# Optimization experiments

Hardware: AMD Instinct MI355X
Metric: run time of the kernel (lower is better)

Reference implementation:

```python
import jax, jax.numpy as jnp
from jax import lax
import numpy as np

NUM_TOKENS = 2048
HIDDEN = 768
MAX_SPAN_WIDTH = 20
NUM_CAND = NUM_TOKENS * MAX_SPAN_WIDTH  # 40960
FEAT = 20
UNARY = 1024
SPAN_DIM = 3 * HIDDEN + FEAT  # 2324
MAX_NUM_SPANS = 512
TOP_SPAN_RATIO = 0.4


def setup_inputs() -> dict:
    key = jax.random.key(0)
    ks = jax.random.split(key, 16)
    starts = jax.random.randint(ks[0], (NUM_CAND,), 0, NUM_TOKENS, dtype=jnp.int32)
    widths = jax.random.randint(ks[1], (NUM_CAND,), 0, MAX_SPAN_WIDTH, dtype=jnp.int32)
    ends = jnp.minimum(starts + widths, NUM_TOKENS - 1)
    p = lambda k, shp: (0.02 * jax.random.normal(k, shp, dtype=jnp.float32))
    return {
        "hidden_states": jax.random.normal(ks[2], (NUM_TOKENS, HIDDEN), dtype=jnp.float32),
        "candidate_starts": starts,
        "candidate_ends": ends,
        "speaker_ids": jax.random.randint(ks[3], (NUM_TOKENS,), 0, 2, dtype=jnp.int32),
        "w_attn": p(ks[4], (HIDDEN,)),
        "b_attn": p(ks[5], ()),
        "W1": p(ks[6], (SPAN_DIM, UNARY)),
        "b1": p(ks[7], (UNARY,)),
        "W2": p(ks[8], (UNARY,)),
        "b2": p(ks[9], ()),
        "emb_width": p(ks[10], (MAX_SPAN_WIDTH, FEAT)),
        "emb_width_prior": p(ks[11], (MAX_SPAN_WIDTH, FEAT)),
        "Wp1": p(ks[12], (FEAT, UNARY)),
        "bp1": p(ks[13], (UNARY,)),
        "Wp2": p(ks[14], (UNARY,)),
        "bp2": p(ks[15], ()),
    }


def extract_spans(starts, ends, scores, num_top, num_words):
    """Greedy NMS-style span pruning: take spans by descending score, rejecting
    spans that partially overlap (cross) an already-accepted span; return
    num_top accepted candidate indices sorted by (start, end)."""
    order = jnp.argsort(-scores)  # descending score
    s_sorted = starts[order]
    e_sorted = ends[order]
    tok = jnp.arange(num_words, dtype=jnp.int32)

    def step(carry, se):
        latest_end, earliest_start, count = carry
        s, e = se
        in_range = (tok >= s) & (tok <= e)
        cross = jnp.any(in_range & (tok > s) & (latest_end > e)) | \
                jnp.any(in_range & (tok < e) & (earliest_start < s))
        accept = jnp.logical_and(~cross, count < num_top)
        latest_end = jnp.where(accept, latest_end.at[s].max(e), latest_end)
        earliest_start = jnp.where(accept, earliest_start.at[e].min(s), earliest_start)
        count = count + accept.astype(jnp.int32)
        return (latest_end, earliest_start, count), accept

    init = (jnp.full((num_words,), -1, jnp.int32),
            jnp.full((num_words,), num_words, jnp.int32),
            jnp.int32(0))
    (_, _, count), accepted = lax.scan(step, init, (s_sorted, e_sorted))
    # sort accepted spans by (start, end); push rejected to the back
    BIG = jnp.int32(np.iinfo(np.int32).max)
    sort_key = jnp.where(accepted, s_sorted * (num_words + 1) + e_sorted, BIG)
    by_pos = jnp.argsort(sort_key)
    picked = order[by_pos[:num_top]]
    # pad (if fewer than num_top accepted) with the first accepted span
    valid = jnp.arange(num_top) < count
    return jnp.where(valid, picked, picked[0])


def reference(hidden_states, candidate_starts, candidate_ends, speaker_ids,
              w_attn, b_attn, W1, b1, W2, b2,
              emb_width, emb_width_prior, Wp1, bp1, Wp2, bp2):
    num_words = hidden_states.shape[0]
    num_top_spans = int(min(MAX_NUM_SPANS, num_words * TOP_SPAN_RATIO))

    # masked softmax attention pooling over each span's tokens
    tok_att = hidden_states @ w_attn + b_attn            # [T]
    doc = jnp.arange(num_words, dtype=jnp.int32)
    token_mask = (doc[None, :] >= candidate_starts[:, None]) & \
                 (doc[None, :] <= candidate_ends[:, None])  # [C, T]
    logits = jnp.where(token_mask, tok_att[None, :], -jnp.inf)
    token_attn = jax.nn.softmax(logits, axis=1)          # [C, T]
    attended = token_attn @ hidden_states                # [C, H]

    width_idx = candidate_ends - candidate_starts        # in [0, MAX_SPAN_WIDTH)
    span_emb = jnp.concatenate([
        hidden_states[candidate_starts],
        hidden_states[candidate_ends],
        emb_width[width_idx],
        attended,
    ], axis=1)                                           # [C, 3H+F]

    h = jax.nn.relu(span_emb @ W1 + b1)
    span_scores = h @ W2 + b2                            # [C]
    hp = jax.nn.relu(emb_width_prior[width_idx] @ Wp1 + bp1)
    span_scores = span_scores + (hp @ Wp2 + bp2)

    pruned_idx = extract_spans(candidate_starts, candidate_ends,
                               lax.stop_gradient(span_scores),
                               num_top_spans, num_words)
    pruned_starts = candidate_starts[pruned_idx]
    pruned_ends = candidate_ends[pruned_idx]
    pruned_emb = span_emb[pruned_idx]
    pruned_scores = span_scores[pruned_idx]
    pruned_speaker_ids = speaker_ids[pruned_starts]
    return (span_emb, pruned_idx, pruned_starts, pruned_ends,
            pruned_emb, pruned_scores, pruned_speaker_ids)
```

## Files before the change

kernel.cpp:

```cpp
#include <hip/hip_runtime.h>
#include <math.h>

#define NT 2048
#define HID 768
#define NC 40960
#define NFEAT 20
#define UN 1024
#define SDIM 2324
#define NTOP 512
#define WMAX 20

#define OFF_IDX   95191040
#define OFF_S     95191552
#define OFF_E     95192064
#define OFF_PEMB  95192576
#define OFF_SC    96382464
#define OFF_SP    96382976

__global__ void k_zero(int* __restrict__ p, int n) {
  int i = blockIdx.x * 256 + threadIdx.x;
  if (i < n) p[i] = 0;
}

__global__ void k_hist(const int* __restrict__ starts, int* __restrict__ hist) {
  int i = blockIdx.x * 256 + threadIdx.x;
  atomicAdd(&hist[starts[i]], 1);
}

__global__ __launch_bounds__(256) void k_prefix(const int* __restrict__ hist,
                                                int* __restrict__ cursor) {
  __shared__ int tsum[256];
  int tid = threadIdx.x;
  int v[8], pre[8];
  int s = 0;
  #pragma unroll
  for (int j = 0; j < 8; ++j) { v[j] = hist[tid * 8 + j]; pre[j] = s; s += v[j]; }
  tsum[tid] = s;
  __syncthreads();
  for (int off = 1; off < 256; off <<= 1) {
    int t = (tid >= off) ? tsum[tid - off] : 0;
    __syncthreads();
    tsum[tid] += t;
    __syncthreads();
  }
  int base = (tid > 0) ? tsum[tid - 1] : 0;
  #pragma unroll
  for (int j = 0; j < 8; ++j) cursor[tid * 8 + j] = base + pre[j];
}

__global__ void k_place(const int* __restrict__ starts, int* __restrict__ cursor,
                        int* __restrict__ ord) {
  int i = blockIdx.x * 256 + threadIdx.x;
  int pos = atomicAdd(&cursor[starts[i]], 1);
  ord[pos] = i;
}

__global__ __launch_bounds__(256) void k_tok_att(const float* __restrict__ hidden,
                                                 const float* __restrict__ w_attn,
                                                 const float* __restrict__ b_attn,
                                                 float* __restrict__ tok_att) {
  int wave = (blockIdx.x * blockDim.x + threadIdx.x) >> 6;
  int lane = threadIdx.x & 63;
  if (wave >= NT) return;
  const float* row = hidden + (size_t)wave * HID;
  float s = 0.f;
  for (int c = lane; c < HID; c += 64) s += row[c] * w_attn[c];
  #pragma unroll
  for (int off = 32; off; off >>= 1) s += __shfl_down(s, off);
  if (lane == 0) tok_att[wave] = s + b_attn[0];
}

__global__ __launch_bounds__(256) void k_pc(const float* __restrict__ emb_width,
                                            const float* __restrict__ W1,
                                            float* __restrict__ Pc) {
  int idx = blockIdx.x * 256 + threadIdx.x;
  int w = idx >> 10, j = idx & 1023;
  float s = 0.f;
  #pragma unroll
  for (int k = 0; k < NFEAT; ++k) s += emb_width[w * NFEAT + k] * W1[(size_t)(2 * HID + k) * UN + j];
  Pc[idx] = s;
}

__global__ __launch_bounds__(256) void k_prior(const float* __restrict__ ewp,
                                               const float* __restrict__ Wp1,
                                               const float* __restrict__ bp1,
                                               const float* __restrict__ Wp2,
                                               const float* __restrict__ bp2,
                                               float* __restrict__ prior) {
  int w = blockIdx.x;
  int tid = threadIdx.x;
  __shared__ float red[256];
  float local = 0.f;
  for (int j = tid; j < UN; j += 256) {
    float hp = bp1[j];
    #pragma unroll
    for (int k = 0; k < NFEAT; ++k) hp += ewp[w * NFEAT + k] * Wp1[k * UN + j];
    local += fmaxf(hp, 0.f) * Wp2[j];
  }
  red[tid] = local;
  __syncthreads();
  for (int st = 128; st > 0; st >>= 1) { if (tid < st) red[tid] += red[tid + st]; __syncthreads(); }
  if (tid == 0) prior[w] = red[0] + bp2[0];
}

__global__ __launch_bounds__(256) void k_matmul_P(const float* __restrict__ hidden,
                                                  const float* __restrict__ W1,
                                                  float* __restrict__ P) {
  __shared__ float As[16][132];
  __shared__ float Bs[16][128];
  int bn = blockIdx.x, bm = blockIdx.y;
  int n0 = bn * 128;
  int seg = n0 >> 10;
  int rowbase = (seg == 0) ? 0 : (seg == 1 ? HID : (2 * HID + NFEAT));
  int j0 = n0 & 1023;
  int tid = threadIdx.x;
  int tx = tid & 15, ty = tid >> 4;
  float acc[8][8] = {};
  for (int k0 = 0; k0 < HID; k0 += 16) {
    #pragma unroll
    for (int q = 0; q < 2; ++q) {
      int idx = q * 256 + tid;
      int m = idx >> 2, kg = idx & 3;
      float4 a = *(const float4*)&hidden[(size_t)(bm * 128 + m) * HID + k0 + kg * 4];
      As[kg * 4 + 0][m] = a.x; As[kg * 4 + 1][m] = a.y;
      As[kg * 4 + 2][m] = a.z; As[kg * 4 + 3][m] = a.w;
      int k = idx >> 5, ng = idx & 31;
      float4 b = *(const float4*)&W1[(size_t)(rowbase + k0 + k) * UN + j0 + ng * 4];
      *(float4*)&Bs[k][ng * 4] = b;
    }
    __syncthreads();
    #pragma unroll
    for (int k = 0; k < 16; ++k) {
      float4 a0 = *(const float4*)&As[k][ty * 8];
      float4 a1 = *(const float4*)&As[k][ty * 8 + 4];
      float4 b0 = *(const float4*)&Bs[k][tx * 8];
      float4 b1 = *(const float4*)&Bs[k][tx * 8 + 4];
      float av[8] = {a0.x, a0.y, a0.z, a0.w, a1.x, a1.y, a1.z, a1.w};
      float bv[8] = {b0.x, b0.y, b0.z, b0.w, b1.x, b1.y, b1.z, b1.w};
      #pragma unroll
      for (int i = 0; i < 8; ++i)
        #pragma unroll
        for (int jj = 0; jj < 8; ++jj) acc[i][jj] += av[i] * bv[jj];
    }
    __syncthreads();
  }
  #pragma unroll
  for (int i = 0; i < 8; ++i) {
    float* prow = &P[(size_t)(bm * 128 + ty * 8 + i) * 3072 + n0 + tx * 8];
    *(float4*)prow = make_float4(acc[i][0], acc[i][1], acc[i][2], acc[i][3]);
    *(float4*)(prow + 4) = make_float4(acc[i][4], acc[i][5], acc[i][6], acc[i][7]);
  }
}

__global__ __launch_bounds__(256) void k_span(
    const int* __restrict__ ord,
    const float* __restrict__ hidden, const int* __restrict__ starts, const int* __restrict__ ends,
    const float* __restrict__ tok_att, const float* __restrict__ emb_width,
    const float* __restrict__ P, const float* __restrict__ Pc,
    const float* __restrict__ b1, const float* __restrict__ W2,
    const float* __restrict__ b2ptr, const float* __restrict__ prior,
    float* __restrict__ out, float* __restrict__ scores, unsigned long long* __restrict__ keys) {
  int i = ord[blockIdx.x];
  int s = starts[i], e = ends[i];
  int w = e - s;
  int L = w + 1;
  int tid = threadIdx.x;
  __shared__ float alpha[WMAX];
  __shared__ float red[256];
  if (tid < 64) {
    float v = (tid < L) ? tok_att[s + tid] : -3.0e38f;
    float m = v;
    #pragma unroll
    for (int off = 32; off; off >>= 1) m = fmaxf(m, __shfl_xor(m, off));
    float ex = (tid < L) ? expf(v - m) : 0.0f;
    float sum = ex;
    #pragma unroll
    for (int off = 32; off; off >>= 1) sum += __shfl_xor(sum, off);
    if (tid < L) alpha[tid] = ex / sum;
  }
  __syncthreads();
  const float* hs = hidden + (size_t)s * HID;
  const float* he = hidden + (size_t)e * HID;
  float* orow = out + (size_t)i * SDIM;
  for (int q = tid; q < SDIM / 4; q += 256) {
    int c = q * 4;
    float4 v;
    if (c < HID) v = *(const float4*)(hs + c);
    else if (c < 2 * HID) v = *(const float4*)(he + (c - HID));
    else if (c < 2 * HID + NFEAT) v = *(const float4*)(emb_width + w * NFEAT + (c - 2 * HID));
    else {
      int cc = c - (2 * HID + NFEAT);
      float ax = 0, ay = 0, az = 0, aw = 0;
      for (int t = 0; t < L; ++t) {
        float a = alpha[t];
        float4 hv = *(const float4*)(hidden + (size_t)(s + t) * HID + cc);
        ax += a * hv.x; ay += a * hv.y; az += a * hv.z; aw += a * hv.w;
      }
      v = make_float4(ax, ay, az, aw);
    }
    *(float4*)(orow + c) = v;
  }
  int j = tid * 4;
  float4 pre = *(const float4*)(b1 + j);
  float4 pa = *(const float4*)(P + (size_t)s * 3072 + j);
  float4 pb = *(const float4*)(P + (size_t)e * 3072 + 1024 + j);
  float4 pc = *(const float4*)(Pc + w * UN + j);
  pre.x += pa.x + pb.x + pc.x;
  pre.y += pa.y + pb.y + pc.y;
  pre.z += pa.z + pb.z + pc.z;
  pre.w += pa.w + pb.w + pc.w;
  for (int t = 0; t < L; ++t) {
    float a = alpha[t];
    float4 pd = *(const float4*)(P + (size_t)(s + t) * 3072 + 2048 + j);
    pre.x += a * pd.x; pre.y += a * pd.y; pre.z += a * pd.z; pre.w += a * pd.w;
  }
  float4 w2 = *(const float4*)(W2 + j);
  float local = fmaxf(pre.x, 0.f) * w2.x + fmaxf(pre.y, 0.f) * w2.y +
                fmaxf(pre.z, 0.f) * w2.z + fmaxf(pre.w, 0.f) * w2.w;
  red[tid] = local;
  __syncthreads();
  for (int st = 128; st > 0; st >>= 1) { if (tid < st) red[tid] += red[tid + st]; __syncthreads(); }
  if (tid == 0) {
    float sc = red[0] + b2ptr[0] + prior[w];
    scores[i] = sc;
    unsigned u = __float_as_uint(sc);
    u = (u >> 31) ? ~u : (u | 0x80000000u);
    unsigned inv = ~u;
    keys[i] = (((unsigned long long)inv) << 32) | (unsigned)i;
  }
}

__global__ __launch_bounds__(256) void k_rank(const unsigned long long* __restrict__ keys,
                                              int* __restrict__ rank) {
  int ic = blockIdx.x >> 5;
  int jc = blockIdx.x & 31;
  int tid = threadIdx.x;
  int ibase = ic * 2048 + tid;
  unsigned long long mk[8];
  int cnt[8];
  #pragma unroll
  for (int k = 0; k < 8; ++k) { mk[k] = keys[ibase + k * 256]; cnt[k] = 0; }
  int j0 = jc * 1280;
  #pragma unroll 4
  for (int j = j0; j < j0 + 1280; ++j) {
    unsigned long long kj = keys[j];
    #pragma unroll
    for (int k = 0; k < 8; ++k) cnt[k] += (kj < mk[k]) ? 1 : 0;
  }
  #pragma unroll
  for (int k = 0; k < 8; ++k) if (cnt[k]) atomicAdd(&rank[ibase + k * 256], cnt[k]);
}

__global__ void k_scatter(const int* __restrict__ rank, int* __restrict__ order) {
  int i = blockIdx.x * 256 + threadIdx.x;
  order[rank[i]] = i;
}

__global__ void k_scan(const int* __restrict__ order,
                       const int* __restrict__ starts,
                       const int* __restrict__ ends,
                       int* __restrict__ acc_idx, int* __restrict__ acc_s,
                       int* __restrict__ acc_e, int* __restrict__ acc_count) {
  __shared__ int LE[NT];
  __shared__ int ES[NT];
  int lane = threadIdx.x;
  for (int t = lane; t < NT; t += 64) { LE[t] = -1; ES[t] = NT; }
  __syncthreads();
  int count = 0;
  for (int base = 0; base < NC && count < NTOP; base += 64) {
    int ci = order[base + lane];
    int sv = starts[ci];
    int ev = ends[ci];
    bool pc = false;
    for (int t = sv; t <= ev; ++t) {
      int l = LE[t], es2 = ES[t];
      pc = pc || ((t > sv) && (l > ev)) || ((t < ev) && (es2 < sv));
    }
    unsigned long long pm = __ballot(pc);
    int localCount = 0;
    int ls = 0, le = -1, li = 0;
    for (int t = 0; t < 64; ++t) {
      int s = __shfl(sv, t);
      int e = __shfl(ev, t);
      int cidx = __shfl(ci, t);
      bool ov = (lane < localCount) &&
                (((s < ls) && (ls <= e) && (e < le)) ||
                 ((ls < s) && (s <= le) && (le < e)));
      bool cross = (((pm >> t) & 1ull) != 0) || __any(ov);
      if (!cross) {
        if (lane == localCount) { ls = s; le = e; li = cidx; }
        localCount++;
        count++;
        if (count >= NTOP) break;
      }
    }
    int cbase = count - localCount;
    if (lane < localCount) {
      acc_idx[cbase + lane] = li;
      acc_s[cbase + lane] = ls;
      acc_e[cbase + lane] = le;
      atomicMax(&LE[ls], le);
      atomicMin(&ES[le], ls);
    }
    __syncthreads();
  }
  if (lane == 0) acc_count[0] = count;
}

__global__ __launch_bounds__(512) void k_outputs(const int* __restrict__ acc_idx,
                                                 const int* __restrict__ acc_s,
                                                 const int* __restrict__ acc_e,
                                                 const int* __restrict__ acc_count,
                                                 const float* __restrict__ scores,
                                                 const int* __restrict__ speaker,
                                                 float* __restrict__ out,
                                                 int* __restrict__ sortedIdx) {
  __shared__ int ks[NTOP];
  int tid = threadIdx.x;
  int count = acc_count[0];
  int key = 0x7FFFFFFF;
  if (tid < count) key = acc_s[tid] * (NT + 1) + acc_e[tid];
  ks[tid] = key;
  __syncthreads();
  if (tid < count) {
    int r = 0;
    for (int b = 0; b < count; ++b) {
      int kb = ks[b];
      r += ((kb < key) || (kb == key && b < tid)) ? 1 : 0;
    }
    int ci = acc_idx[tid];
    out[OFF_IDX + r] = (float)ci;
    out[OFF_S + r]   = (float)acc_s[tid];
    out[OFF_E + r]   = (float)acc_e[tid];
    out[OFF_SC + r]  = scores[ci];
    out[OFF_SP + r]  = (float)speaker[acc_s[tid]];
    sortedIdx[r] = ci;
  }
  __syncthreads();
  if (tid >= count) {
    out[OFF_IDX + tid] = out[OFF_IDX];
    out[OFF_S + tid]   = out[OFF_S];
    out[OFF_E + tid]   = out[OFF_E];
    out[OFF_SC + tid]  = out[OFF_SC];
    out[OFF_SP + tid]  = out[OFF_SP];
    sortedIdx[tid] = sortedIdx[0];
  }
}

__global__ __launch_bounds__(256) void k_copy_emb(const int* __restrict__ sortedIdx,
                                                  float* __restrict__ out) {
  int r = blockIdx.x;
  int ci = sortedIdx[r];
  const float* src = out + (size_t)ci * SDIM;
  float* dst = out + OFF_PEMB + (size_t)r * SDIM;
  for (int q = threadIdx.x; q < SDIM / 4; q += 256) {
    ((float4*)dst)[q] = ((const float4*)src)[q];
  }
}

extern "C" void kernel_launch(void* const* d_in, const int* in_sizes, int n_in,
                              void* d_out, int out_size, void* d_ws, size_t ws_size,
                              hipStream_t stream) {
  const float* hidden   = (const float*)d_in[0];
  const int*   starts   = (const int*)d_in[1];
  const int*   ends     = (const int*)d_in[2];
  const int*   speaker  = (const int*)d_in[3];
  const float* w_attn   = (const float*)d_in[4];
  const float* b_attn   = (const float*)d_in[5];
  const float* W1       = (const float*)d_in[6];
  const float* b1       = (const float*)d_in[7];
  const float* W2       = (const float*)d_in[8];
  const float* b2       = (const float*)d_in[9];
  const float* embw     = (const float*)d_in[10];
  const float* ewp      = (const float*)d_in[11];
  const float* Wp1      = (const float*)d_in[12];
  const float* bp1      = (const float*)d_in[13];
  const float* Wp2      = (const float*)d_in[14];
  const float* bp2      = (const float*)d_in[15];
  float* out = (float*)d_out;

  float* f = (float*)d_ws;
  float* P       = f;
  float* tok_att = P + 6291456;
  float* Pc      = tok_att + 2048;
  float* prior   = Pc + 20480;
  float* scores  = prior + 32;
  unsigned long long* keys = (unsigned long long*)(scores + 40960);
  int* rank      = (int*)(keys + 40960);
  int* order     = rank + 40960;
  int* acc_idx   = order + 40960;
  int* acc_s     = acc_idx + NTOP;
  int* acc_e     = acc_s + NTOP;
  int* acc_count = acc_e + NTOP;
  int* sortedIdx = acc_count + 4;
  int* hist      = sortedIdx + NTOP;
  int* cursor    = hist + NT;
  int* ord       = cursor + NT;

  k_zero<<<dim3(8), dim3(256), 0, stream>>>(hist, NT);
  k_zero<<<dim3(160), dim3(256), 0, stream>>>(rank, NC);
  k_hist<<<dim3(160), dim3(256), 0, stream>>>(starts, hist);
  k_prefix<<<dim3(1), dim3(256), 0, stream>>>(hist, cursor);
  k_place<<<dim3(160), dim3(256), 0, stream>>>(starts, cursor, ord);

  k_tok_att<<<dim3(512), dim3(256), 0, stream>>>(hidden, w_attn, b_attn, tok_att);
  k_pc<<<dim3(80), dim3(256), 0, stream>>>(embw, W1, Pc);
  k_prior<<<dim3(20), dim3(256), 0, stream>>>(ewp, Wp1, bp1, Wp2, bp2, prior);
  k_matmul_P<<<dim3(24, 16), dim3(256), 0, stream>>>(hidden, W1, P);
  k_span<<<dim3(NC), dim3(256), 0, stream>>>(ord, hidden, starts, ends, tok_att, embw, P, Pc,
                                             b1, W2, b2, prior, out, scores, keys);
  k_rank<<<dim3(640), dim3(256), 0, stream>>>(keys, rank);
  k_scatter<<<dim3(160), dim3(256), 0, stream>>>(rank, order);
  k_scan<<<dim3(1), dim3(64), 0, stream>>>(order, starts, ends, acc_idx, acc_s, acc_e, acc_count);
  k_outputs<<<dim3(1), dim3(512), 0, stream>>>(acc_idx, acc_s, acc_e, acc_count, scores,
                                               speaker, out, sortedIdx);
  k_copy_emb<<<dim3(NTOP), dim3(256), 0, stream>>>(sortedIdx, out);
}
```

Measured before the change: 1.031 ms.

## Replace per-span softmax attention sums with double-precision prefix sums

Softmax over each span's tokens is rewritten as ratios of prefix sums of exp(logit)-weighted hidden rows, projected rows and normalizers. These prefix sums are built once in three chunked scan kernels. Each span then reads only two prefix rows instead of looping over up to twenty token rows for both the attended embedding and the projected hidden layer. The block reduction also switches to wave shuffles. The change adds double-precision traffic and large workspaces. Exponentiating without max subtraction risks overflow, and differencing large prefix sums can lose precision.

```diff
diff --git a/kernel.cpp b/kernel.cpp
--- a/kernel.cpp
+++ b/kernel.cpp
@@ -10,6 +10,11 @@
 #define NTOP 512
 #define WMAX 20
 
+#define NCOLS 1793
+#define CHUNK 64
+#define NCHUNK 32
+#define CS_STRIDE 1800
+
 #define OFF_IDX   95191040
 #define OFF_S     95191552
 #define OFF_E     95192064
@@ -58,7 +63,7 @@
 __global__ __launch_bounds__(256) void k_tok_att(const float* __restrict__ hidden,
                                                  const float* __restrict__ w_attn,
                                                  const float* __restrict__ b_attn,
-                                                 float* __restrict__ tok_att) {
+                                                 float* __restrict__ expA) {
   int wave = (blockIdx.x * blockDim.x + threadIdx.x) >> 6;
   int lane = threadIdx.x & 63;
   if (wave >= NT) return;
@@ -67,7 +72,7 @@
   for (int c = lane; c < HID; c += 64) s += row[c] * w_attn[c];
   #pragma unroll
   for (int off = 32; off; off >>= 1) s += __shfl_down(s, off);
-  if (lane == 0) tok_att[wave] = s + b_attn[0];
+  if (lane == 0) expA[wave] = expf(s + b_attn[0]);
 }
 
 __global__ __launch_bounds__(256) void k_pc(const float* __restrict__ emb_width,
@@ -152,10 +157,101 @@
   }
 }
 
+__global__ __launch_bounds__(256) void k_psumA(const float* __restrict__ hidden,
+                                               const float* __restrict__ P,
+                                               const float* __restrict__ expA,
+                                               double* __restrict__ chunkSum) {
+  int col = blockIdx.x * 256 + threadIdx.x;
+  int ch = blockIdx.y;
+  if (col >= NCOLS) return;
+  double acc = 0.0;
+  int t0 = ch * CHUNK;
+  if (col < HID) {
+    const float* p = hidden + col;
+    #pragma unroll 8
+    for (int r = 0; r < CHUNK; ++r) {
+      int t = t0 + r;
+      acc += (double)expA[t] * (double)p[(size_t)t * HID];
+    }
+  } else if (col < HID + UN) {
+    const float* p = P + 2048 + (col - HID);
+    #pragma unroll 8
+    for (int r = 0; r < CHUNK; ++r) {
+      int t = t0 + r;
+      acc += (double)expA[t] * (double)p[(size_t)t * 3072];
+    }
+  } else {
+    #pragma unroll 8
+    for (int r = 0; r < CHUNK; ++r) acc += (double)expA[t0 + r];
+  }
+  chunkSum[(size_t)ch * CS_STRIDE + col] = acc;
+}
+
+__global__ __launch_bounds__(256) void k_psumB(double* __restrict__ chunkSum,
+                                               double* __restrict__ prefH,
+                                               double* __restrict__ prefPd,
+                                               double* __restrict__ prefZ) {
+  int col = blockIdx.x * 256 + threadIdx.x;
+  if (col >= NCOLS) return;
+  double run = 0.0;
+  for (int ch = 0; ch < NCHUNK; ++ch) {
+    size_t o = (size_t)ch * CS_STRIDE + col;
+    double v = chunkSum[o];
+    chunkSum[o] = run;
+    run += v;
+  }
+  if (col < HID) prefH[col] = 0.0;
+  else if (col < HID + UN) prefPd[col - HID] = 0.0;
+  else prefZ[0] = 0.0;
+}
+
+__global__ __launch_bounds__(256) void k_psumC(const float* __restrict__ hidden,
+                                               const float* __restrict__ P,
+                                               const float* __restrict__ expA,
+                                               const double* __restrict__ chunkSum,
+                                               double* __restrict__ prefH,
+                                               double* __restrict__ prefPd,
+                                               double* __restrict__ prefZ) {
+  int col = blockIdx.x * 256 + threadIdx.x;
+  int ch = blockIdx.y;
+  if (col >= NCOLS) return;
+  double acc = chunkSum[(size_t)ch * CS_STRIDE + col];
+  int t0 = ch * CHUNK;
+  if (col < HID) {
+    const float* p = hidden + col;
+    double* o = prefH + col;
+    #pragma unroll 4
+    for (int r = 0; r < CHUNK; ++r) {
+      int t = t0 + r;
+      acc += (double)expA[t] * (double)p[(size_t)t * HID];
+      o[(size_t)(t + 1) * HID] = acc;
+    }
+  } else if (col < HID + UN) {
+    int c = col - HID;
+    const float* p = P + 2048 + c;
+    double* o = prefPd + c;
+    #pragma unroll 4
+    for (int r = 0; r < CHUNK; ++r) {
+      int t = t0 + r;
+      acc += (double)expA[t] * (double)p[(size_t)t * 3072];
+      o[(size_t)(t + 1) * UN] = acc;
+    }
+  } else {
+    #pragma unroll 4
+    for (int r = 0; r < CHUNK; ++r) {
+      int t = t0 + r;
+      acc += (double)expA[t];
+      prefZ[t + 1] = acc;
+    }
+  }
+}
+
 __global__ __launch_bounds__(256) void k_span(
     const int* __restrict__ ord,
     const float* __restrict__ hidden, const int* __restrict__ starts, const int* __restrict__ ends,
-    const float* __restrict__ tok_att, const float* __restrict__ emb_width,
+    const float* __restrict__ emb_width,
+    const double* __restrict__ prefH, const double* __restrict__ prefPd,
+    const double* __restrict__ prefZ,
     const float* __restrict__ P, const float* __restrict__ Pc,
     const float* __restrict__ b1, const float* __restrict__ W2,
     const float* __restrict__ b2ptr, const float* __restrict__ prior,
@@ -163,24 +259,12 @@
   int i = ord[blockIdx.x];
   int s = starts[i], e = ends[i];
   int w = e - s;
-  int L = w + 1;
   int tid = threadIdx.x;
-  __shared__ float alpha[WMAX];
-  __shared__ float red[256];
-  if (tid < 64) {
-    float v = (tid < L) ? tok_att[s + tid] : -3.0e38f;
-    float m = v;
-    #pragma unroll
-    for (int off = 32; off; off >>= 1) m = fmaxf(m, __shfl_xor(m, off));
-    float ex = (tid < L) ? expf(v - m) : 0.0f;
-    float sum = ex;
-    #pragma unroll
-    for (int off = 32; off; off >>= 1) sum += __shfl_xor(sum, off);
-    if (tid < L) alpha[tid] = ex / sum;
-  }
-  __syncthreads();
+  double invZ = 1.0 / (prefZ[e + 1] - prefZ[s]);
   const float* hs = hidden + (size_t)s * HID;
   const float* he = hidden + (size_t)e * HID;
+  const double* pHs = prefH + (size_t)s * HID;
+  const double* pHe = prefH + (size_t)(e + 1) * HID;
   float* orow = out + (size_t)i * SDIM;
   for (int q = tid; q < SDIM / 4; q += 256) {
     int c = q * 4;
@@ -190,13 +274,12 @@
     else if (c < 2 * HID + NFEAT) v = *(const float4*)(emb_width + w * NFEAT + (c - 2 * HID));
     else {
       int cc = c - (2 * HID + NFEAT);
-      float ax = 0, ay = 0, az = 0, aw = 0;
-      for (int t = 0; t < L; ++t) {
-        float a = alpha[t];
-        float4 hv = *(const float4*)(hidden + (size_t)(s + t) * HID + cc);
-        ax += a * hv.x; ay += a * hv.y; az += a * hv.z; aw += a * hv.w;
-      }
-      v = make_float4(ax, ay, az, aw);
+      const double* pe = pHe + cc;
+      const double* ps = pHs + cc;
+      v = make_float4((float)((pe[0] - ps[0]) * invZ),
+                      (float)((pe[1] - ps[1]) * invZ),
+                      (float)((pe[2] - ps[2]) * invZ),
+                      (float)((pe[3] - ps[3]) * invZ));
     }
     *(float4*)(orow + c) = v;
   }
@@ -205,23 +288,22 @@
   float4 pa = *(const float4*)(P + (size_t)s * 3072 + j);
   float4 pb = *(const float4*)(P + (size_t)e * 3072 + 1024 + j);
   float4 pc = *(const float4*)(Pc + w * UN + j);
-  pre.x += pa.x + pb.x + pc.x;
-  pre.y += pa.y + pb.y + pc.y;
-  pre.z += pa.z + pb.z + pc.z;
-  pre.w += pa.w + pb.w + pc.w;
-  for (int t = 0; t < L; ++t) {
-    float a = alpha[t];
-    float4 pd = *(const float4*)(P + (size_t)(s + t) * 3072 + 2048 + j);
-    pre.x += a * pd.x; pre.y += a * pd.y; pre.z += a * pd.z; pre.w += a * pd.w;
-  }
+  const double* pds = prefPd + (size_t)s * UN + j;
+  const double* pde = prefPd + (size_t)(e + 1) * UN + j;
+  pre.x += pa.x + pb.x + pc.x + (float)((pde[0] - pds[0]) * invZ);
+  pre.y += pa.y + pb.y + pc.y + (float)((pde[1] - pds[1]) * invZ);
+  pre.z += pa.z + pb.z + pc.z + (float)((pde[2] - pds[2]) * invZ);
+  pre.w += pa.w + pb.w + pc.w + (float)((pde[3] - pds[3]) * invZ);
   float4 w2 = *(const float4*)(W2 + j);
   float local = fmaxf(pre.x, 0.f) * w2.x + fmaxf(pre.y, 0.f) * w2.y +
                 fmaxf(pre.z, 0.f) * w2.z + fmaxf(pre.w, 0.f) * w2.w;
-  red[tid] = local;
+  #pragma unroll
+  for (int off = 32; off; off >>= 1) local += __shfl_down(local, off);
+  __shared__ float red[4];
+  if ((tid & 63) == 0) red[tid >> 6] = local;
   __syncthreads();
-  for (int st = 128; st > 0; st >>= 1) { if (tid < st) red[tid] += red[tid + st]; __syncthreads(); }
   if (tid == 0) {
-    float sc = red[0] + b2ptr[0] + prior[w];
+    float sc = red[0] + red[1] + red[2] + red[3] + b2ptr[0] + prior[w];
     scores[i] = sc;
     unsigned u = __float_as_uint(sc);
     u = (u >> 31) ? ~u : (u | 0x80000000u);
@@ -381,12 +463,16 @@
 
   float* f = (float*)d_ws;
   float* P       = f;
-  float* tok_att = P + 6291456;
-  float* Pc      = tok_att + 2048;
+  float* expA    = P + 6291456;
+  float* Pc      = expA + 2048;
   float* prior   = Pc + 20480;
   float* scores  = prior + 32;
   unsigned long long* keys = (unsigned long long*)(scores + 40960);
-  int* rank      = (int*)(keys + 40960);
+  double* prefPd = (double*)(keys + 40960);
+  double* prefZ  = prefPd + 2049 * 1024;
+  double* chunkSum = prefZ + 2056;
+  double* prefH  = chunkSum + 32 * CS_STRIDE;
+  int* rank      = (int*)(prefH + 2049 * 768);
   int* order     = rank + 40960;
   int* acc_idx   = order + 40960;
   int* acc_s     = acc_idx + NTOP;
@@ -403,11 +489,18 @@
   k_prefix<<<dim3(1), dim3(256), 0, stream>>>(hist, cursor);
   k_place<<<dim3(160), dim3(256), 0, stream>>>(starts, cursor, ord);
 
-  k_tok_att<<<dim3(512), dim3(256), 0, stream>>>(hidden, w_attn, b_attn, tok_att);
+  k_tok_att<<<dim3(512), dim3(256), 0, stream>>>(hidden, w_attn, b_attn, expA);
   k_pc<<<dim3(80), dim3(256), 0, stream>>>(embw, W1, Pc);
   k_prior<<<dim3(20), dim3(256), 0, stream>>>(ewp, Wp1, bp1, Wp2, bp2, prior);
   k_matmul_P<<<dim3(24, 16), dim3(256), 0, stream>>>(hidden, W1, P);
-  k_span<<<dim3(NC), dim3(256), 0, stream>>>(ord, hidden, starts, ends, tok_att, embw, P, Pc,
+
+  k_psumA<<<dim3(8, NCHUNK), dim3(256), 0, stream>>>(hidden, P, expA, chunkSum);
+  k_psumB<<<dim3(8), dim3(256), 0, stream>>>(chunkSum, prefH, prefPd, prefZ);
+  k_psumC<<<dim3(8, NCHUNK), dim3(256), 0, stream>>>(hidden, P, expA, chunkSum,
+                                                     prefH, prefPd, prefZ);
+
+  k_span<<<dim3(NC), dim3(256), 0, stream>>>(ord, hidden, starts, ends, embw,
+                                             prefH, prefPd, prefZ, P, Pc,
                                              b1, W2, b2, prior, out, scores, keys);
   k_rank<<<dim3(640), dim3(256), 0, stream>>>(keys, rank);
   k_scatter<<<dim3(160), dim3(256), 0, stream>>>(rank, order);
```

Result: no change. 1.042 ms (+1.1%).
